# Performance work log

Measured on AMD Instinct MI355X. Metric: run time of the kernel, lower is better.

## Reference

```python
import jax, jax.numpy as jnp
import numpy as np

H = W = 17
C = 4
DN = ('NCHW', 'OIHW', 'NCHW')

_SCENT = jnp.array([[[[0.0, 0.125, 0.25, 0.125, 0.0],
                      [0.125, 0.25, 0.5, 0.25, 0.125],
                      [0.25, 0.5, 1.0, 0.5, 0.25],
                      [0.125, 0.25, 0.5, 0.25, 0.125],
                      [0.0, 0.125, 0.25, 0.125, 0.0]]]], dtype=jnp.float32)  # [1,1,5,5]

_DX = (jnp.outer(jnp.array([1.0, 2.0, 1.0]), jnp.array([-1.0, 0.0, 1.0])) / 8.0).astype(jnp.float32)  # [3,3]
_DY = _DX.T


def _maxpool3(x):  # [B,1,H,W] -> [B,1,H,W], 3x3 stride 1, pad 1
    return jax.lax.reduce_window(x, -jnp.inf, jax.lax.max,
                                 (1, 1, 3, 3), (1, 1, 1, 1),
                                 ((0, 0), (0, 0), (1, 1), (1, 1)))


def _depthwise3(x, k):  # x:[B,4,H,W], k:[3,3] applied per-channel
    k4 = jnp.broadcast_to(k, (C, 1, 3, 3))
    return jax.lax.conv_general_dilated(x, k4, (1, 1), ((1, 1), (1, 1)),
                                        dimension_numbers=DN, feature_group_count=C)


def setup_inputs() -> dict:
    key = jax.random.key(0)
    k1, k2, k3, k4 = jax.random.split(key, 4)
    B = 16384
    return {
        'cell': jax.random.uniform(k1, (B, C, H, W), dtype=jnp.float32),
        'food': jax.random.uniform(k2, (B, H, W), dtype=jnp.float32),
        'w3': jax.random.normal(k3, (16, 12, 1, 1), dtype=jnp.float32) * 0.1,
        'b3': jnp.zeros((16,), dtype=jnp.float32),
        'w4': jax.random.normal(k4, (4, 16, 1, 1), dtype=jnp.float32) * 0.1,
        'b4': jnp.zeros((4,), dtype=jnp.float32),
        'steps': 32,
    }


def reference(cell, food, w3, b3, w4, b4, steps):
    # Scent field depends only on food -> compute once (same value every step).
    scent = jax.lax.conv_general_dilated(food[:, None], _SCENT, (1, 1),
                                         ((2, 2), (2, 2)), dimension_numbers=DN)[:, 0]

    w3m = w3[:, :, 0, 0]  # [16,12]
    w4m = w4[:, :, 0, 0]  # [4,16]

    def step(c, _):
        x = c.at[:, 3].set(scent)                      # in-place scent write (as in torch)
        pre = _maxpool3(x[:, 0:1]) > 0.1               # [B,1,H,W] bool
        y1 = _depthwise3(x, _DX)
        y2 = _depthwise3(x, _DY)
        y = jnp.concatenate((x, y1, y2), axis=1)       # [B,12,H,W]
        h = jax.nn.relu(jnp.einsum('bchw,oc->bohw', y, w3m) + b3[None, :, None, None])
        d = jnp.einsum('bchw,oc->bohw', h, w4m) + b4[None, :, None, None]
        xn = x + d                                     # residual on scent-updated cell
        post = _maxpool3(xn[:, 0:1]) > 0.1
        life = (pre & post).astype(xn.dtype)           # [B,1,H,W] broadcast over channels
        xn = jnp.clip(xn * life, -10.0, 10.0)
        return xn, None

    cell, _ = jax.lax.scan(step, cell, None, length=steps)
    ch0 = cell[:, 0:1]
    living_count = ch0.sum(axis=(1, 2, 3))
    living_above = (ch0 > 0.1).astype(jnp.float32).sum(axis=(1, 2, 3))
    return cell, food, living_count, living_above
```

## Files before the change

kernel.cpp:

```cpp
#include <hip/hip_runtime.h>
#include <hip/hip_fp16.h>

#define HW 17
#define NPIX 289

typedef float f2 __attribute__((ext_vector_type(2)));

__device__ __forceinline__ float bperm(int a, float v) {
    return __int_as_float(__builtin_amdgcn_ds_bpermute(a, __float_as_int(v)));
}
__device__ __forceinline__ float max3f(float a, float b, float c){ return fmaxf(fmaxf(a,b),c); }
__device__ __forceinline__ float clampf(float v){ return fminf(fmaxf(v,-10.f),10.f); }
__device__ __forceinline__ f2 mk2(float s){ return (f2){s,s}; }
__device__ __forceinline__ unsigned h2u(__half2 h){ union{__half2 h; unsigned u;} v; v.h=h; return v.u; }
__device__ __forceinline__ __half2 u2h(unsigned u){ union{__half2 h; unsigned u;} v; v.u=u; return v.h; }

#define EL(A,c) (A[(c)>>1][(c)&1])

#define SOBWIN(XA, vL, dL, sxp, syp)                                          \
    {                                                                         \
        float v[2*NC+2], d[2*NC+2];                                           \
        v[0] = (vL); d[0] = (dL);                                             \
        _Pragma("unroll")                                                     \
        for (int i = 1; i < 2*NC+2; ++i) {                                    \
            const int c = 2*CP0 - 1 + i;                                      \
            if (c <= 16) {                                                    \
                const float xv = EL(XA, c);                                   \
                const float u_ = bperm(upA, xv), dn_ = bperm(dnA, xv);        \
                v[i] = u_ + 2.f*xv + dn_; d[i] = dn_ - u_;                    \
            } else { v[i] = 0.f; d[i] = 0.f; }                                \
        }                                                                     \
        (vL) = v[2*NC]; (dL) = d[2*NC];                                       \
        _Pragma("unroll")                                                     \
        for (int q = 0; q < NC; ++q) {                                        \
            sxp[q] = (f2){ 0.125f*(v[2*q+2]-v[2*q]),                          \
                           0.125f*(v[2*q+3]-v[2*q+1]) };                      \
            syp[q] = (f2){ 0.125f*(d[2*q] + 2.f*d[2*q+1] + d[2*q+2]),         \
                           0.125f*(d[2*q+1] + 2.f*d[2*q+2] + d[2*q+3]) };     \
        }                                                                     \
    }

#define CA_CHUNK(P0_, P1_)                                                    \
{                                                                             \
    constexpr int CP0 = (P0_);                                                \
    constexpr int NC  = (P1_) - (P0_);                                        \
    f2 sxp0[NC], syp0[NC], sxp1[NC], syp1[NC], sxp2[NC], syp2[NC];            \
    SOBWIN(X0, vL0, dL0, sxp0, syp0)                                          \
    SOBWIN(X1, vL1, dL1, sxp1, syp1)                                          \
    SOBWIN(X2, vL2, dL2, sxp2, syp2)                                          \
    f2 scl[NC], s3x[NC], s3y[NC];                                             \
    _Pragma("unroll")                                                         \
    for (int q = 0; q < NC; ++q) {                                            \
        const int jp = CP0 + q;                                               \
        const float2 sf = __half22float2(u2h(ldsP[lb + 17 + jp]));            \
        scl[q] = (f2){ sf.x, sf.y };                                          \
        const float2 a = __half22float2(u2h(ldsP[lb + 2*jp]));                \
        if (2*jp + 1 <= 16) {                                                 \
            const float2 bq = __half22float2(u2h(ldsP[lb + 2*jp + 1]));       \
            s3x[q] = (f2){ a.x, bq.x }; s3y[q] = (f2){ a.y, bq.y };           \
        } else {                                                              \
            s3x[q] = (f2){ a.x, 0.f }; s3y[q] = (f2){ a.y, 0.f };             \
        }                                                                     \
    }                                                                         \
    f2 dacc0[NC], dacc1[NC], dacc2[NC], dacc3[NC];                            \
    _Pragma("unroll")                                                         \
    for (int q = 0; q < NC; ++q) {                                            \
        dacc0[q] = mk2(b4[0]); dacc1[q] = mk2(b4[1]);                         \
        dacc2[q] = mk2(b4[2]); dacc3[q] = mk2(b4[3]);                         \
    }                                                                         \
    _Pragma("clang loop unroll_count(2)")                                     \
    for (int o = 0; o < 16; ++o) {                                            \
        const float wx0 = w3[o*12+0], wx1 = w3[o*12+1], wx2 = w3[o*12+2], wx3 = w3[o*12+3]; \
        const float wa0 = w3[o*12+4], wa1 = w3[o*12+5], wa2 = w3[o*12+6], wa3 = w3[o*12+7]; \
        const float wb0 = w3[o*12+8], wb1 = w3[o*12+9], wb2 = w3[o*12+10], wb3 = w3[o*12+11]; \
        const float bo = b3[o];                                               \
        const float u0 = w4[o], u1 = w4[16+o], u2 = w4[32+o], u3 = w4[48+o];  \
        _Pragma("unroll")                                                     \
        for (int q = 0; q < NC; ++q) {                                        \
            const int jp = CP0 + q;                                           \
            f2 h = mk2(bo);                                                   \
            h += mk2(wx0) * X0[jp];  h += mk2(wx1) * X1[jp];                  \
            h += mk2(wx2) * X2[jp];  h += mk2(wx3) * scl[q];                  \
            h += mk2(wa0) * sxp0[q]; h += mk2(wa1) * sxp1[q];                 \
            h += mk2(wa2) * sxp2[q]; h += mk2(wa3) * s3x[q];                  \
            h += mk2(wb0) * syp0[q]; h += mk2(wb1) * syp1[q];                 \
            h += mk2(wb2) * syp2[q]; h += mk2(wb3) * s3y[q];                  \
            h.x = fmaxf(h.x, 0.f); h.y = fmaxf(h.y, 0.f);                     \
            dacc0[q] += mk2(u0) * h; dacc1[q] += mk2(u1) * h;                 \
            dacc2[q] += mk2(u2) * h; dacc3[q] += mk2(u3) * h;                 \
        }                                                                     \
    }                                                                         \
    _Pragma("unroll")                                                         \
    for (int q = 0; q < NC; ++q) {                                            \
        const int jp = CP0 + q;                                               \
        X0[jp] = (X0[jp] + dacc0[q]) * am2;                                   \
        X1[jp] = (X1[jp] + dacc1[q]) * am2;                                   \
        X2[jp] = (X2[jp] + dacc2[q]) * am2;                                   \
        X3[jp] = (scl[q] + dacc3[q]) * am2;                                   \
    }                                                                         \
}

__global__ __launch_bounds__(256)
void ca_kernel(const float* __restrict__ cell, const float* __restrict__ food,
               const float* __restrict__ w3, const float* __restrict__ b3,
               const float* __restrict__ w4, const float* __restrict__ b4,
               const int* __restrict__ steps_p, const int B,
               float* __restrict__ out_cell, float* __restrict__ out_food,
               float* __restrict__ out_cnt, float* __restrict__ out_abv)
{
    __shared__ unsigned ldsP[256 * 29];
    const int t    = threadIdx.x;
    const int lb   = t * 29;
    const int lane = t & 63;
    const int wid  = blockIdx.x * (blockDim.x >> 6) + (t >> 6);
    const int bl   = lane / 17;
    const int r    = lane - bl * 17;
    const int batch = wid * 3 + bl;
    const bool active = (bl < 3) && (batch < B);
    const float am = active ? 1.f : 0.f;
    const f2 am2 = mk2(am);

    const int upA  = ((r >= 1)            ? (lane - 1) : 63) << 2;
    const int dnA  = ((r <= 15 && bl < 3) ? (lane + 1) : 63) << 2;
    const int up2A = ((r >= 2)            ? (lane - 2) : 63) << 2;
    const int dn2A = ((r <= 14 && bl < 3) ? (lane + 2) : 63) << 2;

    const size_t fbase = (size_t)(active ? batch : 0) * NPIX + (size_t)r * HW;
    float f[HW];
    #pragma unroll
    for (int c = 0; c < HW; ++c) f[c] = active ? food[fbase + c] : 0.f;
    #pragma unroll
    for (int c = 0; c < HW; ++c) if (active) out_food[fbase + c] = f[c];

    {
        float hf[HW];
        #pragma unroll
        for (int c = 0; c < HW; ++c) {
            float s = f[c];
            if (c >= 1)  s += 0.5f  * f[c - 1];
            if (c <= 15) s += 0.5f  * f[c + 1];
            if (c >= 2)  s += 0.25f * f[c - 2];
            if (c <= 14) s += 0.25f * f[c + 2];
            hf[c] = s;
        }
        float sc[HW];
        {
            float fu2[HW], fd2[HW];
            #pragma unroll
            for (int c = 0; c < HW; ++c) {
                float u1 = bperm(upA, hf[c]),  d1 = bperm(dnA, hf[c]);
                float u2 = bperm(up2A, hf[c]), d2 = bperm(dn2A, hf[c]);
                sc[c] = hf[c] + 0.5f * (u1 + d1) + 0.25f * (u2 + d2);
                fu2[c] = bperm(up2A, f[c]);
                fd2[c] = bperm(dn2A, f[c]);
            }
            #pragma unroll
            for (int c = 0; c < HW; ++c) {
                float corr = 0.f;
                if (c >= 2)  corr += fu2[c - 2] + fd2[c - 2];
                if (c <= 14) corr += fu2[c + 2] + fd2[c + 2];
                sc[c] = (sc[c] - 0.0625f * corr) * am;
            }
        }
        {
            float vS[HW + 2], dS[HW + 2];
            vS[0] = 0.f; vS[HW + 1] = 0.f; dS[0] = 0.f; dS[HW + 1] = 0.f;
            #pragma unroll
            for (int c = 0; c < HW; ++c) {
                float u = bperm(upA, sc[c]), d = bperm(dnA, sc[c]);
                vS[c + 1] = u + 2.f * sc[c] + d;
                dS[c + 1] = d - u;
            }
            #pragma unroll
            for (int c = 0; c < HW; ++c) {
                float sx3 = 0.125f * (vS[c + 2] - vS[c]);
                float sy3 = 0.125f * (dS[c] + 2.f * dS[c + 1] + dS[c + 2]);
                ldsP[lb + c] = h2u(__floats2half2_rn(sx3, sy3));
            }
        }
        #pragma unroll
        for (int i = 0; i < 9; ++i)
            ldsP[lb + 17 + i] =
                h2u(__floats2half2_rn(sc[2 * i], (2 * i + 1 < HW) ? sc[2 * i + 1] : 0.f));
    }

    const size_t cb = (size_t)(active ? batch : 0) * (4 * NPIX) + (size_t)r * HW;
    f2 X0[9], X1[9], X2[9], X3[9];
    #pragma unroll
    for (int c = 0; c < HW; ++c) {
        EL(X0, c) = active ? cell[cb + c] : 0.f;
        EL(X1, c) = active ? cell[cb + NPIX + c] : 0.f;
        EL(X2, c) = active ? cell[cb + 2 * NPIX + c] : 0.f;
        EL(X3, c) = active ? cell[cb + 3 * NPIX + c] : 0.f;
    }
    X0[8].y = 0.f; X1[8].y = 0.f; X2[8].y = 0.f; X3[8].y = 0.f;

    const int steps = steps_p[0];
    for (int s = 0; s < steps; ++s) {
        unsigned pmask = 0u;
        {
            float rm[HW];
            #pragma unroll
            for (int c = 0; c < HW; ++c) {
                float a  = (c >= 1)  ? EL(X0, c - 1) : 0.f;
                float b2 = (c <= 15) ? EL(X0, c + 1) : 0.f;
                rm[c] = max3f(a, EL(X0, c), b2);
            }
            #pragma unroll
            for (int c = 0; c < HW; ++c) {
                float pm = max3f(rm[c], bperm(upA, rm[c]), bperm(dnA, rm[c]));
                pmask |= (pm > 0.1f) ? (1u << c) : 0u;
            }
        }

        float vL0 = 0.f, dL0 = 0.f, vL1 = 0.f, dL1 = 0.f, vL2 = 0.f, dL2 = 0.f;
        CA_CHUNK(0, 3)
        CA_CHUNK(3, 6)
        CA_CHUNK(6, 9)
        X0[8].y = 0.f; X1[8].y = 0.f; X2[8].y = 0.f; X3[8].y = 0.f;

        {
            float rm[HW];
            #pragma unroll
            for (int c = 0; c < HW; ++c) {
                float a  = (c >= 1)  ? EL(X0, c - 1) : 0.f;
                float b2 = (c <= 15) ? EL(X0, c + 1) : 0.f;
                rm[c] = max3f(a, EL(X0, c), b2);
            }
            #pragma unroll
            for (int c = 0; c < HW; ++c) {
                float pm = max3f(rm[c], bperm(upA, rm[c]), bperm(dnA, rm[c]));
                const bool L = ((pmask & (1u << c)) != 0u) && (pm > 0.1f);
                EL(X0, c) = L ? clampf(EL(X0, c)) : 0.f;
                EL(X1, c) = L ? clampf(EL(X1, c)) : 0.f;
                EL(X2, c) = L ? clampf(EL(X2, c)) : 0.f;
                EL(X3, c) = L ? clampf(EL(X3, c)) : 0.f;
            }
        }
    }

    #pragma unroll
    for (int c = 0; c < HW; ++c) {
        if (active) {
            out_cell[cb + c]            = EL(X0, c);
            out_cell[cb + NPIX + c]     = EL(X1, c);
            out_cell[cb + 2 * NPIX + c] = EL(X2, c);
            out_cell[cb + 3 * NPIX + c] = EL(X3, c);
        }
    }

    float rs = 0.f, rc = 0.f;
    #pragma unroll
    for (int c = 0; c < HW; ++c) {
        const float v = EL(X0, c);
        rs += v;
        rc += (v > 0.1f) ? 1.f : 0.f;
    }
    float ssum = rs, scnt = rc;
    for (int k = 1; k <= 16; ++k) {
        int a = ((lane + k) & 63) << 2;
        ssum += bperm(a, rs);
        scnt += bperm(a, rc);
    }
    if (active && r == 0) { out_cnt[batch] = ssum; out_abv[batch] = scnt; }
}

extern "C" void kernel_launch(void* const* d_in, const int* in_sizes, int n_in,
                              void* d_out, int out_size, void* d_ws, size_t ws_size,
                              hipStream_t stream) {
    const float* cell  = (const float*)d_in[0];
    const float* food  = (const float*)d_in[1];
    const float* w3    = (const float*)d_in[2];
    const float* b3    = (const float*)d_in[3];
    const float* w4    = (const float*)d_in[4];
    const float* b4    = (const float*)d_in[5];
    const int*   steps = (const int*)d_in[6];

    const int B = in_sizes[0] / (4 * NPIX);

    float* out      = (float*)d_out;
    float* out_cell = out;
    float* out_food = out      + (size_t)B * 4 * NPIX;
    float* out_cnt  = out_food + (size_t)B * NPIX;
    float* out_abv  = out_cnt  + (size_t)B;

    const int waves  = (B + 2) / 3;
    const int blocks = (waves + 3) / 4;
    hipLaunchKernelGGL(ca_kernel, dim3(blocks), dim3(256), 0, stream,
                       cell, food, w3, b3, w4, b4, steps, B,
                       out_cell, out_food, out_cnt, out_abv);
}
```

Before: 2.030 ms.

## Store channel 3 as packed fp16 and add occupancy launch bound

Result: slower. 2.572 ms (+26.7%).

```diff
diff --git a/kernel.cpp b/kernel.cpp
--- a/kernel.cpp
+++ b/kernel.cpp
@@ -5,6 +5,7 @@
 #define NPIX 289
 
 typedef float f2 __attribute__((ext_vector_type(2)));
+typedef __fp16 h2v __attribute__((ext_vector_type(2)));
 
 __device__ __forceinline__ float bperm(int a, float v) {
     return __int_as_float(__builtin_amdgcn_ds_bpermute(a, __float_as_int(v)));
@@ -14,6 +15,9 @@
 __device__ __forceinline__ f2 mk2(float s){ return (f2){s,s}; }
 __device__ __forceinline__ unsigned h2u(__half2 h){ union{__half2 h; unsigned u;} v; v.h=h; return v.u; }
 __device__ __forceinline__ __half2 u2h(unsigned u){ union{__half2 h; unsigned u;} v; v.u=u; return v.h; }
+__device__ __forceinline__ unsigned packrtz(float a, float b){
+    union{h2v h; unsigned u;} v; v.h = __builtin_amdgcn_cvt_pkrtz(a, b); return v.u;
+}
 
 #define EL(A,c) (A[(c)>>1][(c)&1])
 
@@ -96,11 +100,11 @@
         X0[jp] = (X0[jp] + dacc0[q]) * am2;                                   \
         X1[jp] = (X1[jp] + dacc1[q]) * am2;                                   \
         X2[jp] = (X2[jp] + dacc2[q]) * am2;                                   \
-        X3[jp] = (scl[q] + dacc3[q]) * am2;                                   \
+        X3h[jp] = packrtz(scl[q].x + dacc3[q].x, scl[q].y + dacc3[q].y);      \
     }                                                                         \
 }
 
-__global__ __launch_bounds__(256)
+__global__ __launch_bounds__(256, 4)
 void ca_kernel(const float* __restrict__ cell, const float* __restrict__ food,
                const float* __restrict__ w3, const float* __restrict__ b3,
                const float* __restrict__ w4, const float* __restrict__ b4,
@@ -185,15 +189,18 @@
     }
 
     const size_t cb = (size_t)(active ? batch : 0) * (4 * NPIX) + (size_t)r * HW;
-    f2 X0[9], X1[9], X2[9], X3[9];
+    f2 X0[9], X1[9], X2[9];
+    unsigned X3h[9];
+    unsigned Lmask = 0u;
     #pragma unroll
     for (int c = 0; c < HW; ++c) {
         EL(X0, c) = active ? cell[cb + c] : 0.f;
         EL(X1, c) = active ? cell[cb + NPIX + c] : 0.f;
         EL(X2, c) = active ? cell[cb + 2 * NPIX + c] : 0.f;
-        EL(X3, c) = active ? cell[cb + 3 * NPIX + c] : 0.f;
-    }
-    X0[8].y = 0.f; X1[8].y = 0.f; X2[8].y = 0.f; X3[8].y = 0.f;
+    }
+    X0[8].y = 0.f; X1[8].y = 0.f; X2[8].y = 0.f;
+    #pragma unroll
+    for (int i = 0; i < 9; ++i) X3h[i] = 0u;
 
     const int steps = steps_p[0];
     for (int s = 0; s < steps; ++s) {
@@ -214,10 +221,12 @@
         }
 
         float vL0 = 0.f, dL0 = 0.f, vL1 = 0.f, dL1 = 0.f, vL2 = 0.f, dL2 = 0.f;
-        CA_CHUNK(0, 3)
-        CA_CHUNK(3, 6)
-        CA_CHUNK(6, 9)
-        X0[8].y = 0.f; X1[8].y = 0.f; X2[8].y = 0.f; X3[8].y = 0.f;
+        CA_CHUNK(0, 2)
+        CA_CHUNK(2, 4)
+        CA_CHUNK(4, 6)
+        CA_CHUNK(6, 8)
+        CA_CHUNK(8, 9)
+        X0[8].y = 0.f; X1[8].y = 0.f; X2[8].y = 0.f;
 
         {
             float rm[HW];
@@ -227,15 +236,17 @@
                 float b2 = (c <= 15) ? EL(X0, c + 1) : 0.f;
                 rm[c] = max3f(a, EL(X0, c), b2);
             }
+            unsigned lm = 0u;
             #pragma unroll
             for (int c = 0; c < HW; ++c) {
                 float pm = max3f(rm[c], bperm(upA, rm[c]), bperm(dnA, rm[c]));
                 const bool L = ((pmask & (1u << c)) != 0u) && (pm > 0.1f);
+                lm |= L ? (1u << c) : 0u;
                 EL(X0, c) = L ? clampf(EL(X0, c)) : 0.f;
                 EL(X1, c) = L ? clampf(EL(X1, c)) : 0.f;
                 EL(X2, c) = L ? clampf(EL(X2, c)) : 0.f;
-                EL(X3, c) = L ? clampf(EL(X3, c)) : 0.f;
-            }
+            }
+            Lmask = lm;
         }
     }
 
@@ -245,7 +256,15 @@
             out_cell[cb + c]            = EL(X0, c);
             out_cell[cb + NPIX + c]     = EL(X1, c);
             out_cell[cb + 2 * NPIX + c] = EL(X2, c);
-            out_cell[cb + 3 * NPIX + c] = EL(X3, c);
+            float x3v;
+            if (steps == 0) {
+                x3v = cell[cb + 3 * NPIX + c];
+            } else {
+                const float2 p = __half22float2(u2h(X3h[c >> 1]));
+                const float raw = (c & 1) ? p.y : p.x;
+                x3v = ((Lmask >> c) & 1u) ? clampf(raw) : 0.f;
+            }
+            out_cell[cb + 3 * NPIX + c] = x3v;
         }
     }
 
```

## Skip channel-3 update except on final step, stash it in LDS

Applied to the files above, without the earlier changes.

After: 2.210 ms. +8.9%, slower.

```diff
diff --git a/kernel.cpp b/kernel.cpp
--- a/kernel.cpp
+++ b/kernel.cpp
@@ -3,17 +3,25 @@
 
 #define HW 17
 #define NPIX 289
+#define LSTRIDE 39
+#define LOFF_SXY 0
+#define LOFF_SC  17
+#define LOFF_X3  26
 
 typedef float f2 __attribute__((ext_vector_type(2)));
+typedef __fp16 h2v __attribute__((ext_vector_type(2)));
 
 __device__ __forceinline__ float bperm(int a, float v) {
     return __int_as_float(__builtin_amdgcn_ds_bpermute(a, __float_as_int(v)));
 }
 __device__ __forceinline__ float max3f(float a, float b, float c){ return fmaxf(fmaxf(a,b),c); }
-__device__ __forceinline__ float clampf(float v){ return fminf(fmaxf(v,-10.f),10.f); }
+__device__ __forceinline__ float clampf(float v){ return __builtin_amdgcn_fmed3f(v, -10.f, 10.f); }
 __device__ __forceinline__ f2 mk2(float s){ return (f2){s,s}; }
 __device__ __forceinline__ unsigned h2u(__half2 h){ union{__half2 h; unsigned u;} v; v.h=h; return v.u; }
 __device__ __forceinline__ __half2 u2h(unsigned u){ union{__half2 h; unsigned u;} v; v.u=u; return v.h; }
+__device__ __forceinline__ unsigned packrtz(float a, float b){
+    union{h2v h; unsigned u;} v; v.h = __builtin_amdgcn_cvt_pkrtz(a, b); return v.u;
+}
 
 #define EL(A,c) (A[(c)>>1][(c)&1])
 
@@ -40,6 +48,19 @@
         }                                                                     \
     }
 
+#define LOAD_CONST(q, jp)                                                     \
+        const float2 sf = __half22float2(u2h(ldsP[lb + LOFF_SC + (jp)]));     \
+        scl[q] = (f2){ sf.x, sf.y };                                          \
+        {                                                                     \
+            const float2 a_ = __half22float2(u2h(ldsP[lb + LOFF_SXY + 2*(jp)])); \
+            if (2*(jp) + 1 <= 16) {                                           \
+                const float2 b_ = __half22float2(u2h(ldsP[lb + LOFF_SXY + 2*(jp) + 1])); \
+                s3x[q] = (f2){ a_.x, b_.x }; s3y[q] = (f2){ a_.y, b_.y };     \
+            } else {                                                          \
+                s3x[q] = (f2){ a_.x, 0.f }; s3y[q] = (f2){ a_.y, 0.f };       \
+            }                                                                 \
+        }
+
 #define CA_CHUNK(P0_, P1_)                                                    \
 {                                                                             \
     constexpr int CP0 = (P0_);                                                \
@@ -50,23 +71,11 @@
     SOBWIN(X2, vL2, dL2, sxp2, syp2)                                          \
     f2 scl[NC], s3x[NC], s3y[NC];                                             \
     _Pragma("unroll")                                                         \
+    for (int q = 0; q < NC; ++q) { LOAD_CONST(q, CP0 + q) }                   \
+    f2 dacc0[NC], dacc1[NC], dacc2[NC];                                       \
+    _Pragma("unroll")                                                         \
     for (int q = 0; q < NC; ++q) {                                            \
-        const int jp = CP0 + q;                                               \
-        const float2 sf = __half22float2(u2h(ldsP[lb + 17 + jp]));            \
-        scl[q] = (f2){ sf.x, sf.y };                                          \
-        const float2 a = __half22float2(u2h(ldsP[lb + 2*jp]));                \
-        if (2*jp + 1 <= 16) {                                                 \
-            const float2 bq = __half22float2(u2h(ldsP[lb + 2*jp + 1]));       \
-            s3x[q] = (f2){ a.x, bq.x }; s3y[q] = (f2){ a.y, bq.y };           \
-        } else {                                                              \
-            s3x[q] = (f2){ a.x, 0.f }; s3y[q] = (f2){ a.y, 0.f };             \
-        }                                                                     \
-    }                                                                         \
-    f2 dacc0[NC], dacc1[NC], dacc2[NC], dacc3[NC];                            \
-    _Pragma("unroll")                                                         \
-    for (int q = 0; q < NC; ++q) {                                            \
-        dacc0[q] = mk2(b4[0]); dacc1[q] = mk2(b4[1]);                         \
-        dacc2[q] = mk2(b4[2]); dacc3[q] = mk2(b4[3]);                         \
+        dacc0[q] = mk2(b4[0]); dacc1[q] = mk2(b4[1]); dacc2[q] = mk2(b4[2]);  \
     }                                                                         \
     _Pragma("clang loop unroll_count(2)")                                     \
     for (int o = 0; o < 16; ++o) {                                            \
@@ -74,7 +83,7 @@
         const float wa0 = w3[o*12+4], wa1 = w3[o*12+5], wa2 = w3[o*12+6], wa3 = w3[o*12+7]; \
         const float wb0 = w3[o*12+8], wb1 = w3[o*12+9], wb2 = w3[o*12+10], wb3 = w3[o*12+11]; \
         const float bo = b3[o];                                               \
-        const float u0 = w4[o], u1 = w4[16+o], u2 = w4[32+o], u3 = w4[48+o];  \
+        const float u0 = w4[o], u1 = w4[16+o], u2 = w4[32+o];                 \
         _Pragma("unroll")                                                     \
         for (int q = 0; q < NC; ++q) {                                        \
             const int jp = CP0 + q;                                           \
@@ -87,7 +96,7 @@
             h += mk2(wb2) * syp2[q]; h += mk2(wb3) * s3y[q];                  \
             h.x = fmaxf(h.x, 0.f); h.y = fmaxf(h.y, 0.f);                     \
             dacc0[q] += mk2(u0) * h; dacc1[q] += mk2(u1) * h;                 \
-            dacc2[q] += mk2(u2) * h; dacc3[q] += mk2(u3) * h;                 \
+            dacc2[q] += mk2(u2) * h;                                          \
         }                                                                     \
     }                                                                         \
     _Pragma("unroll")                                                         \
@@ -96,7 +105,97 @@
         X0[jp] = (X0[jp] + dacc0[q]) * am2;                                   \
         X1[jp] = (X1[jp] + dacc1[q]) * am2;                                   \
         X2[jp] = (X2[jp] + dacc2[q]) * am2;                                   \
-        X3[jp] = (scl[q] + dacc3[q]) * am2;                                   \
+    }                                                                         \
+}
+
+#define CH3_CHUNK(P0_, P1_)                                                   \
+{                                                                             \
+    constexpr int CP0 = (P0_);                                                \
+    constexpr int NC  = (P1_) - (P0_);                                        \
+    f2 sxp0[NC], syp0[NC], sxp1[NC], syp1[NC], sxp2[NC], syp2[NC];            \
+    SOBWIN(X0, wL0, eL0, sxp0, syp0)                                          \
+    SOBWIN(X1, wL1, eL1, sxp1, syp1)                                          \
+    SOBWIN(X2, wL2, eL2, sxp2, syp2)                                          \
+    f2 scl[NC], s3x[NC], s3y[NC];                                             \
+    _Pragma("unroll")                                                         \
+    for (int q = 0; q < NC; ++q) { LOAD_CONST(q, CP0 + q) }                   \
+    f2 dacc3[NC];                                                             \
+    _Pragma("unroll")                                                         \
+    for (int q = 0; q < NC; ++q) dacc3[q] = mk2(b4[3]);                       \
+    for (int o = 0; o < 16; ++o) {                                            \
+        const float wx0 = w3[o*12+0], wx1 = w3[o*12+1], wx2 = w3[o*12+2], wx3 = w3[o*12+3]; \
+        const float wa0 = w3[o*12+4], wa1 = w3[o*12+5], wa2 = w3[o*12+6], wa3 = w3[o*12+7]; \
+        const float wb0 = w3[o*12+8], wb1 = w3[o*12+9], wb2 = w3[o*12+10], wb3 = w3[o*12+11]; \
+        const float bo = b3[o];                                               \
+        const float u3 = w4[48+o];                                            \
+        _Pragma("unroll")                                                     \
+        for (int q = 0; q < NC; ++q) {                                        \
+            const int jp = CP0 + q;                                           \
+            f2 h = mk2(bo);                                                   \
+            h += mk2(wx0) * X0[jp];  h += mk2(wx1) * X1[jp];                  \
+            h += mk2(wx2) * X2[jp];  h += mk2(wx3) * scl[q];                  \
+            h += mk2(wa0) * sxp0[q]; h += mk2(wa1) * sxp1[q];                 \
+            h += mk2(wa2) * sxp2[q]; h += mk2(wa3) * s3x[q];                  \
+            h += mk2(wb0) * syp0[q]; h += mk2(wb1) * syp1[q];                 \
+            h += mk2(wb2) * syp2[q]; h += mk2(wb3) * s3y[q];                  \
+            h.x = fmaxf(h.x, 0.f); h.y = fmaxf(h.y, 0.f);                     \
+            dacc3[q] += mk2(u3) * h;                                          \
+        }                                                                     \
+    }                                                                         \
+    _Pragma("unroll")                                                         \
+    for (int q = 0; q < NC; ++q) {                                            \
+        const int jp = CP0 + q;                                               \
+        ldsP[lb + LOFF_X3 + jp] = packrtz(scl[q].x + dacc3[q].x,              \
+                                          scl[q].y + dacc3[q].y);             \
+    }                                                                         \
+}
+
+#define PREMASK                                                               \
+{                                                                             \
+    float rm[HW];                                                             \
+    _Pragma("unroll")                                                         \
+    for (int c = 0; c < HW; ++c) {                                            \
+        float a  = (c >= 1)  ? EL(X0, c - 1) : 0.f;                           \
+        float b2 = (c <= 15) ? EL(X0, c + 1) : 0.f;                           \
+        rm[c] = max3f(a, EL(X0, c), b2);                                      \
+    }                                                                         \
+    pmask = 0u;                                                               \
+    _Pragma("unroll")                                                         \
+    for (int c = 0; c < HW; ++c) {                                            \
+        float pm = max3f(rm[c], bperm(upA, rm[c]), bperm(dnA, rm[c]));        \
+        pmask |= (pm > 0.1f) ? (1u << c) : 0u;                                \
+    }                                                                         \
+}
+
+#define CHUNKS5                                                               \
+{                                                                             \
+    float vL0 = 0.f, dL0 = 0.f, vL1 = 0.f, dL1 = 0.f, vL2 = 0.f, dL2 = 0.f;   \
+    CA_CHUNK(0, 2) CA_CHUNK(2, 4) CA_CHUNK(4, 6) CA_CHUNK(6, 8) CA_CHUNK(8, 9)\
+    X0[8].y = 0.f; X1[8].y = 0.f; X2[8].y = 0.f;                              \
+}
+
+#define GATE(W3)                                                              \
+{                                                                             \
+    float rm[HW];                                                             \
+    _Pragma("unroll")                                                         \
+    for (int c = 0; c < HW; ++c) {                                            \
+        float a  = (c >= 1)  ? EL(X0, c - 1) : 0.f;                           \
+        float b2 = (c <= 15) ? EL(X0, c + 1) : 0.f;                           \
+        rm[c] = max3f(a, EL(X0, c), b2);                                      \
+    }                                                                         \
+    _Pragma("unroll")                                                         \
+    for (int c = 0; c < HW; ++c) {                                            \
+        float pm = max3f(rm[c], bperm(upA, rm[c]), bperm(dnA, rm[c]));        \
+        const bool L = ((pmask & (1u << c)) != 0u) && (pm > 0.1f);            \
+        const float Lf = L ? 1.f : 0.f;                                       \
+        EL(X0, c) = clampf(EL(X0, c)) * Lf;                                   \
+        EL(X1, c) = clampf(EL(X1, c)) * Lf;                                   \
+        EL(X2, c) = clampf(EL(X2, c)) * Lf;                                   \
+        if (W3) {                                                             \
+            const float2 p = __half22float2(u2h(ldsP[lb + LOFF_X3 + (c >> 1)])); \
+            const float raw = (c & 1) ? p.y : p.x;                            \
+            if (active) out_cell[cb + 3 * NPIX + c] = clampf(raw) * Lf;       \
+        }                                                                     \
     }                                                                         \
 }
 
@@ -108,9 +207,9 @@
                float* __restrict__ out_cell, float* __restrict__ out_food,
                float* __restrict__ out_cnt, float* __restrict__ out_abv)
 {
-    __shared__ unsigned ldsP[256 * 29];
+    __shared__ unsigned ldsP[256 * LSTRIDE];
     const int t    = threadIdx.x;
-    const int lb   = t * 29;
+    const int lb   = t * LSTRIDE;
     const int lane = t & 63;
     const int wid  = blockIdx.x * (blockDim.x >> 6) + (t >> 6);
     const int bl   = lane / 17;
@@ -175,68 +274,42 @@
             for (int c = 0; c < HW; ++c) {
                 float sx3 = 0.125f * (vS[c + 2] - vS[c]);
                 float sy3 = 0.125f * (dS[c] + 2.f * dS[c + 1] + dS[c + 2]);
-                ldsP[lb + c] = h2u(__floats2half2_rn(sx3, sy3));
+                ldsP[lb + LOFF_SXY + c] = h2u(__floats2half2_rn(sx3, sy3));
             }
         }
         #pragma unroll
         for (int i = 0; i < 9; ++i)
-            ldsP[lb + 17 + i] =
+            ldsP[lb + LOFF_SC + i] =
                 h2u(__floats2half2_rn(sc[2 * i], (2 * i + 1 < HW) ? sc[2 * i + 1] : 0.f));
     }
 
     const size_t cb = (size_t)(active ? batch : 0) * (4 * NPIX) + (size_t)r * HW;
-    f2 X0[9], X1[9], X2[9], X3[9];
+    f2 X0[9], X1[9], X2[9];
     #pragma unroll
     for (int c = 0; c < HW; ++c) {
         EL(X0, c) = active ? cell[cb + c] : 0.f;
         EL(X1, c) = active ? cell[cb + NPIX + c] : 0.f;
         EL(X2, c) = active ? cell[cb + 2 * NPIX + c] : 0.f;
-        EL(X3, c) = active ? cell[cb + 3 * NPIX + c] : 0.f;
-    }
-    X0[8].y = 0.f; X1[8].y = 0.f; X2[8].y = 0.f; X3[8].y = 0.f;
+    }
+    X0[8].y = 0.f; X1[8].y = 0.f; X2[8].y = 0.f;
 
     const int steps = steps_p[0];
-    for (int s = 0; s < steps; ++s) {
-        unsigned pmask = 0u;
+    unsigned pmask;
+
+    for (int s = 0; s < steps - 1; ++s) {
+        PREMASK
+        CHUNKS5
+        GATE(0)
+    }
+
+    if (steps > 0) {
+        PREMASK
         {
-            float rm[HW];
-            #pragma unroll
-            for (int c = 0; c < HW; ++c) {
-                float a  = (c >= 1)  ? EL(X0, c - 1) : 0.f;
-                float b2 = (c <= 15) ? EL(X0, c + 1) : 0.f;
-                rm[c] = max3f(a, EL(X0, c), b2);
-            }
-            #pragma unroll
-            for (int c = 0; c < HW; ++c) {
-                float pm = max3f(rm[c], bperm(upA, rm[c]), bperm(dnA, rm[c]));
-                pmask |= (pm > 0.1f) ? (1u << c) : 0u;
-            }
-        }
-
-        float vL0 = 0.f, dL0 = 0.f, vL1 = 0.f, dL1 = 0.f, vL2 = 0.f, dL2 = 0.f;
-        CA_CHUNK(0, 3)
-        CA_CHUNK(3, 6)
-        CA_CHUNK(6, 9)
-        X0[8].y = 0.f; X1[8].y = 0.f; X2[8].y = 0.f; X3[8].y = 0.f;
-
-        {
-            float rm[HW];
-            #pragma unroll
-            for (int c = 0; c < HW; ++c) {
-                float a  = (c >= 1)  ? EL(X0, c - 1) : 0.f;
-                float b2 = (c <= 15) ? EL(X0, c + 1) : 0.f;
-                rm[c] = max3f(a, EL(X0, c), b2);
-            }
-            #pragma unroll
-            for (int c = 0; c < HW; ++c) {
-                float pm = max3f(rm[c], bperm(upA, rm[c]), bperm(dnA, rm[c]));
-                const bool L = ((pmask & (1u << c)) != 0u) && (pm > 0.1f);
-                EL(X0, c) = L ? clampf(EL(X0, c)) : 0.f;
-                EL(X1, c) = L ? clampf(EL(X1, c)) : 0.f;
-                EL(X2, c) = L ? clampf(EL(X2, c)) : 0.f;
-                EL(X3, c) = L ? clampf(EL(X3, c)) : 0.f;
-            }
-        }
+            float wL0 = 0.f, eL0 = 0.f, wL1 = 0.f, eL1 = 0.f, wL2 = 0.f, eL2 = 0.f;
+            CH3_CHUNK(0, 2) CH3_CHUNK(2, 4) CH3_CHUNK(4, 6) CH3_CHUNK(6, 8) CH3_CHUNK(8, 9)
+        }
+        CHUNKS5
+        GATE(1)
     }
 
     #pragma unroll
@@ -245,7 +318,7 @@
             out_cell[cb + c]            = EL(X0, c);
             out_cell[cb + NPIX + c]     = EL(X1, c);
             out_cell[cb + 2 * NPIX + c] = EL(X2, c);
-            out_cell[cb + 3 * NPIX + c] = EL(X3, c);
+            if (steps == 0) out_cell[cb + 3 * NPIX + c] = cell[cb + 3 * NPIX + c];
         }
     }
 
```
